# Optimization experiments

Measured on AMD Instinct MI355X. Metric: run time of the kernel, lower is better.

The kernel has to match this reference:

```python
import jax, jax.numpy as jnp
from jax import lax
import numpy as np

B, N, NPOINT, NSAMPLE = 4, 8192, 1024, 32
RADIUS = 0.2
EPS = 1e-5
C_IN = 16
MLP_DIMS = [(3 + C_IN, 64), (64, 64), (64, 128)]


def setup_inputs() -> dict:
    key = jax.random.key(0)
    ks = jax.random.split(key, 16)
    inp = {
        "xyz": jax.random.uniform(ks[0], (B, N, 3), dtype=jnp.float32),
        "points": jax.random.normal(ks[1], (B, N, C_IN), dtype=jnp.float32),
    }
    for i, (cin, cout) in enumerate(MLP_DIMS, 1):
        inp[f"w{i}"] = jax.random.normal(ks[1 + i], (cout, cin), dtype=jnp.float32) / np.sqrt(cin)
        inp[f"b{i}"] = jnp.zeros((cout,), jnp.float32)
        inp[f"g{i}"] = jnp.ones((cout,), jnp.float32)
        inp[f"be{i}"] = jnp.zeros((cout,), jnp.float32)
    return inp


def fps(xyz, npoint):
    # Farthest point sampling; sequential by nature -> lax.scan over npoint steps.
    # Deterministic start at index 0 (torch version uses a random start).
    b, n, _ = xyz.shape
    def step(carry, _):
        dist, far = carry
        centroid = jnp.take_along_axis(xyz, far[:, None, None], axis=1)  # [B,1,3]
        d = jnp.sum((xyz - centroid) ** 2, -1)                            # [B,N]
        dist = jnp.minimum(dist, d)
        return (dist, jnp.argmax(dist, -1).astype(jnp.int32)), far
    init = (jnp.full((b, n), 1e10, xyz.dtype), jnp.zeros((b,), jnp.int32))
    _, idxs = lax.scan(step, init, None, length=npoint)
    return jnp.transpose(idxs)  # [B, npoint]


def gather2(pts, idx):  # pts [B,N,C], idx [B,S] -> [B,S,C]
    return jnp.take_along_axis(pts, idx[..., None], axis=1)


def gather3(pts, idx):  # pts [B,N,C], idx [B,S,K] -> [B,S,K,C]
    b, s, k = idx.shape
    out = jnp.take_along_axis(pts, idx.reshape(b, s * k)[..., None], axis=1)
    return out.reshape(b, s, k, pts.shape[-1])


def ball_query(radius, nsample, xyz, new_xyz):
    n = xyz.shape[1]
    # [B,S,N] pairwise squared distances (the memory-bound hot spot)
    sqr = jnp.sum((new_xyz[:, :, None, :] - xyz[:, None, :, :]) ** 2, -1)
    gidx = jnp.where(sqr > radius * radius, n, jnp.arange(n, dtype=jnp.int32))
    gidx = jnp.sort(gidx, axis=-1)[:, :, :nsample]
    first = gidx[:, :, :1]
    return jnp.where(gidx == n, first, gidx)


def mlp_layer(x, w, b, g, be):
    # 1x1 Conv2d + BatchNorm2d (train mode: batch stats over B,S,K) + ReLU
    y = jnp.einsum('bskc,oc->bsko', x, w) + b
    mu = jnp.mean(y, axis=(0, 1, 2))
    var = jnp.var(y, axis=(0, 1, 2))
    y = (y - mu) * (g * lax.rsqrt(var + EPS)) + be
    return jax.nn.relu(y)


def reference(xyz, points, w1, b1, g1, be1, w2, b2, g2, be2, w3, b3, g3, be3):
    fps_idx = fps(xyz, NPOINT)                       # [B,S]
    new_xyz = gather2(xyz, fps_idx)                  # [B,S,3]
    idx = ball_query(RADIUS, NSAMPLE, xyz, new_xyz)  # [B,S,K]
    grouped_xyz_norm = gather3(xyz, idx) - new_xyz[:, :, None, :]  # [B,S,K,3]
    grouped_points = gather3(points, idx)            # [B,S,K,C]
    feat = jnp.concatenate([grouped_xyz_norm, grouped_points], -1)  # [B,S,K,3+C]
    feat = mlp_layer(feat, w1, b1, g1, be1)
    feat = mlp_layer(feat, w2, b2, g2, be2)
    feat = mlp_layer(feat, w3, b3, g3, be3)
    new_points = jnp.max(feat, axis=2)               # max-pool over neighbors -> [B,S,128]
    return new_xyz, new_points
```

## Files before the change

### kernel.cpp

```cpp
#include <hip/hip_runtime.h>

#define NB 4
#define NP 8192
#define NS 1024
#define NK 32
#define CNT_ALL 131072.0f

typedef float v2f __attribute__((ext_vector_type(2)));

template <int CTRL>
__device__ __forceinline__ unsigned dpp_max_u32(unsigned m)
{
    unsigned o = (unsigned)__builtin_amdgcn_update_dpp((int)m, (int)m, CTRL, 0xF, 0xF, false);
    return (o > m) ? o : m;
}

template <int CTRL>
__device__ __forceinline__ unsigned long long dpp_max_u64(unsigned long long k)
{
    unsigned lo = (unsigned)k, hi = (unsigned)(k >> 32);
    unsigned olo = (unsigned)__builtin_amdgcn_update_dpp((int)lo, (int)lo, CTRL, 0xF, 0xF, false);
    unsigned ohi = (unsigned)__builtin_amdgcn_update_dpp((int)hi, (int)hi, CTRL, 0xF, 0xF, false);
    unsigned long long o = ((unsigned long long)ohi << 32) | (unsigned long long)olo;
    return (o > k) ? o : k;
}

__global__ __launch_bounds__(512, 2) void fps_kernel(const float* __restrict__ xyz,
                                                     float* __restrict__ newxyz,
                                                     float* __restrict__ st)
{
#pragma clang fp contract(off)
    if (blockIdx.x >= NB) {
        for (int i = threadIdx.x; i < 4096; i += 512) st[i] = 0.f;
        return;
    }
    const int b = blockIdx.x;
    const int tid = threadIdx.x;
    const int lane = tid & 63;
    const int w = tid >> 6;
    const float* xb = xyz + (size_t)b * NP * 3;

    __shared__ float4 s_p4[NP];
    __shared__ unsigned long long s_kv[2][8];

#pragma unroll
    for (int k = 0; k < 16; ++k) {
        const int i = k * 512 + tid;
        s_p4[i] = make_float4(xb[3 * i + 0], xb[3 * i + 1], xb[3 * i + 2], 0.f);
    }
    __syncthreads();

    v2f px[8], py[8], pz[8], dist[8];
    const int base = tid << 4;
#pragma unroll
    for (int m = 0; m < 8; ++m) {
        const int p0 = base + 2 * m;
        const float4 a = s_p4[p0];
        const float4 c = s_p4[p0 + 1];
        px[m] = v2f{a.x, c.x};
        py[m] = v2f{a.y, c.y};
        pz[m] = v2f{a.z, c.z};
        dist[m] = v2f{1e10f, 1e10f};
    }
    float cx = s_p4[0].x, cy = s_p4[0].y, cz = s_p4[0].z;
    float* ob = newxyz + (size_t)b * NS * 3;

    for (int it = 0; it < NS; ++it) {
        if (tid == 0) { ob[it * 3 + 0] = cx; ob[it * 3 + 1] = cy; ob[it * 3 + 2] = cz; }
        const v2f cxx = v2f{cx, cx}, cyy = v2f{cy, cy}, czz = v2f{cz, cz};
        v2f bdv = v2f{-1.0f, -1.0f};
#pragma unroll
        for (int m = 0; m < 8; ++m) {
            v2f dx = px[m] - cxx, dy = py[m] - cyy, dz = pz[m] - czz;
            v2f d = (dx * dx + dy * dy) + dz * dz;
            v2f dj = __builtin_elementwise_min(dist[m], d);
            dist[m] = dj;
            bdv = __builtin_elementwise_max(bdv, dj);
        }
        const float bd = fmaxf(bdv.x, bdv.y);
        const unsigned ub = __float_as_uint(bd);
        unsigned m0 = dpp_max_u32<0xB1>(ub);
        m0 = dpp_max_u32<0x4E>(m0);
        m0 = dpp_max_u32<0x141>(m0);
        m0 = dpp_max_u32<0x140>(m0);
        m0 = dpp_max_u32<0x142>(m0);
        m0 = dpp_max_u32<0x143>(m0);
        const unsigned maxbits = (unsigned)__builtin_amdgcn_readlane((int)m0, 63);
        const unsigned long long bm = __ballot(ub == maxbits);
        const int srclane = __ffsll(bm) - 1;
        if (lane == srclane) {
            int j = 0;
#pragma unroll
            for (int m = 7; m >= 0; --m) {
                if (dist[m].y == bd) j = 2 * m + 1;
                if (dist[m].x == bd) j = 2 * m;
            }
            const int wbi = base + j;
            s_kv[it & 1][w] = ((unsigned long long)maxbits << 32)
                            | (unsigned)(NP - 1 - wbi);
        }
        __syncthreads();
        unsigned long long kv = s_kv[it & 1][lane & 7];
        kv = dpp_max_u64<0xB1>(kv);
        kv = dpp_max_u64<0x4E>(kv);
        kv = dpp_max_u64<0x141>(kv);
        const int fi = NP - 1 - (int)(unsigned)(kv & 0xFFFFFFFFull);
        const float4 c4 = s_p4[fi];
        cx = c4.x; cy = c4.y; cz = c4.z;
    }
}

__device__ __forceinline__ void bn_coef(const float* __restrict__ sums,
                                        const float* __restrict__ sqs,
                                        const float* __restrict__ g,
                                        const float* __restrict__ be,
                                        int C, int c, float& sc, float& sh)
{
    float s = 0.f, q = 0.f;
#pragma unroll
    for (int k = 0; k < 8; ++k) { s += sums[k * C + c]; q += sqs[k * C + c]; }
    const float mean = s / CNT_ALL;
    const float var = q / CNT_ALL - mean * mean;
    sc = g[c] / sqrtf(var + 1e-5f);
    sh = be[c] - mean * sc;
}

__global__ __launch_bounds__(256) void phaseA_kernel(
    const float* __restrict__ xyz, const float* __restrict__ pts,
    const float* __restrict__ newxyz,
    const float* __restrict__ w1, const float* __restrict__ b1,
    float* __restrict__ y1, float* __restrict__ st)
{
    __shared__ int   s_ball[8][NK];
    __shared__ float s_feat[256][20];
    __shared__ float s_ps[256], s_pq[256];
    float* sums1 = st;
    float* sqs1 = st + 512;

    const int tid = threadIdx.x;
    const int bk = blockIdx.x;
    const int lane = tid & 63;
    const int wv_id = tid >> 6;

    const int b = (8 * bk) >> 10;
    const float* xb = xyz + (size_t)b * NP * 3;
    const float rr = (float)(0.2 * 0.2);
    for (int r = 0; r < 2; ++r) {
        const int lg = 2 * wv_id + r;
        const int sg = 8 * bk + lg;
        const float cx = newxyz[sg * 3 + 0];
        const float cy = newxyz[sg * 3 + 1];
        const float cz = newxyz[sg * 3 + 2];
        int cnt = 0;
        for (int base = 0; base < NP && cnt < NK; base += 64) {
            const int p = base + lane;
            float dx = xb[p * 3 + 0] - cx;
            float dy = xb[p * 3 + 1] - cy;
            float dz = xb[p * 3 + 2] - cz;
            float d = __fadd_rn(__fadd_rn(__fmul_rn(dx, dx), __fmul_rn(dy, dy)),
                                __fmul_rn(dz, dz));
            bool in = (d <= rr);
            unsigned long long mask = __ballot(in);
            int before = __popcll(mask & ((1ull << lane) - 1ull));
            int pos = cnt + before;
            if (in && pos < NK) s_ball[lg][pos] = p;
            cnt += (int)__popcll(mask);
        }
        cnt = min(cnt, NK);
        const int v0 = s_ball[lg][0];
        if (lane < NK && lane >= cnt) s_ball[lg][lane] = v0;
    }
    __syncthreads();
    {
        const int lg = tid >> 5, k = tid & 31;
        const int id = s_ball[lg][k];
        const int sg = 8 * bk + lg;
        const float* pp = xyz + ((size_t)b * NP + id) * 3;
        const float* cp = newxyz + (size_t)sg * 3;
        float* f = s_feat[tid];
        f[0] = pp[0] - cp[0];
        f[1] = pp[1] - cp[1];
        f[2] = pp[2] - cp[2];
        const float4* q4 = (const float4*)(pts + ((size_t)b * NP + id) * 16);
#pragma unroll
        for (int i = 0; i < 4; ++i) {
            float4 v = q4[i];
            f[3 + 4 * i + 0] = v.x; f[3 + 4 * i + 1] = v.y;
            f[3 + 4 * i + 2] = v.z; f[3 + 4 * i + 3] = v.w;
        }
        f[19] = 0.f;
    }
    __syncthreads();
    const int c = tid & 63, rg = tid >> 6;
    float wv[20];
#pragma unroll
    for (int j = 0; j < 19; ++j) wv[j] = w1[c * 19 + j];
    wv[19] = 0.f;
    const float bs = b1[c];
    float s = 0.f, q = 0.f;
    for (int r = 0; r < 64; ++r) {
        const int row = rg * 64 + r;
        const float4* f4 = (const float4*)s_feat[row];
        float acc = bs;
#pragma unroll
        for (int j4 = 0; j4 < 5; ++j4) {
            float4 v = f4[j4];
            acc += wv[4*j4+0]*v.x + wv[4*j4+1]*v.y + wv[4*j4+2]*v.z + wv[4*j4+3]*v.w;
        }
        y1[((size_t)256 * bk + row) * 64 + c] = acc;
        s += acc; q += acc * acc;
    }
    s_ps[tid] = s; s_pq[tid] = q;
    __syncthreads();
    if (rg == 0) {
        float ts = s_ps[c] + s_ps[64 + c] + s_ps[128 + c] + s_ps[192 + c];
        float tq = s_pq[c] + s_pq[64 + c] + s_pq[128 + c] + s_pq[192 + c];
        atomicAdd(&sums1[(bk & 7) * 64 + c], ts);
        atomicAdd(&sqs1[(bk & 7) * 64 + c], tq);
    }
}

__global__ __launch_bounds__(256) void phaseB_kernel(
    const float* __restrict__ y1,
    const float* __restrict__ g1, const float* __restrict__ be1,
    const float* __restrict__ w2, const float* __restrict__ b2,
    float* __restrict__ y2, float* __restrict__ st)
{
    __shared__ float x_lds[128 * 64];
    __shared__ float s_sc[64], s_sh[64];
    __shared__ float s_ps[256], s_pq[256];
    const float* sums1 = st;
    const float* sqs1 = st + 512;
    float* sums2 = st + 1024;
    float* sqs2 = st + 1536;

    const int tid = threadIdx.x;
    const int bk = blockIdx.x;
    if (tid < 64) {
        float sc, sh;
        bn_coef(sums1, sqs1, g1, be1, 64, tid, sc, sh);
        s_sc[tid] = sc; s_sh[tid] = sh;
    }
    __syncthreads();
    const int c = tid & 63, rg = tid >> 6;
    float wv[64];
#pragma unroll
    for (int j = 0; j < 64; ++j) wv[j] = w2[c * 64 + j];
    const float bs = b2[c];
    float s = 0.f, q = 0.f;
    for (int half = 0; half < 2; ++half) {
        const size_t row0 = (size_t)256 * bk + 128 * half;
        const float4* y1g = (const float4*)(y1 + row0 * 64);
        float4* xl4 = (float4*)x_lds;
#pragma unroll
        for (int i = 0; i < 8; ++i) {
            const int slot = i * 256 + tid;
            float4 v = y1g[slot];
            const int c4 = (slot & 15) * 4;
            float4 o;
            o.x = fmaxf(v.x * s_sc[c4+0] + s_sh[c4+0], 0.f);
            o.y = fmaxf(v.y * s_sc[c4+1] + s_sh[c4+1], 0.f);
            o.z = fmaxf(v.z * s_sc[c4+2] + s_sh[c4+2], 0.f);
            o.w = fmaxf(v.w * s_sc[c4+3] + s_sh[c4+3], 0.f);
            xl4[slot] = o;
        }
        __syncthreads();
        for (int r = 0; r < 32; ++r) {
            const int row = rg * 32 + r;
            const float4* x4 = (const float4*)(x_lds + row * 64);
            float acc = bs;
#pragma unroll
            for (int j4 = 0; j4 < 16; ++j4) {
                float4 v = x4[j4];
                acc += wv[4*j4+0]*v.x + wv[4*j4+1]*v.y + wv[4*j4+2]*v.z + wv[4*j4+3]*v.w;
            }
            y2[(row0 + row) * 64 + c] = acc;
            s += acc; q += acc * acc;
        }
        __syncthreads();
    }
    s_ps[tid] = s; s_pq[tid] = q;
    __syncthreads();
    if (rg == 0) {
        float ts = s_ps[c] + s_ps[64 + c] + s_ps[128 + c] + s_ps[192 + c];
        float tq = s_pq[c] + s_pq[64 + c] + s_pq[128 + c] + s_pq[192 + c];
        atomicAdd(&sums2[(bk & 7) * 64 + c], ts);
        atomicAdd(&sqs2[(bk & 7) * 64 + c], tq);
    }
}

__global__ __launch_bounds__(256) void phaseC_kernel(
    const float* __restrict__ y2,
    const float* __restrict__ g2, const float* __restrict__ be2,
    const float* __restrict__ w3, const float* __restrict__ b3,
    float* __restrict__ st)
{
    __shared__ float s_x[NK * 64];
    __shared__ float s_sc[64], s_sh[64];
    __shared__ float s_p3s[256], s_p3q[256];
    const float* sums2 = st + 1024;
    const float* sqs2 = st + 1536;
    float* sums3 = st + 2048;
    float* sqs3 = st + 3072;

    const int tid = threadIdx.x;
    const int bk = blockIdx.x;
    if (tid < 64) {
        float sc, sh;
        bn_coef(sums2, sqs2, g2, be2, 64, tid, sc, sh);
        s_sc[tid] = sc; s_sh[tid] = sh;
    }
    __syncthreads();
    const int c = tid & 127, rg = tid >> 7;
    float wv[64];
#pragma unroll
    for (int j = 0; j < 64; ++j) wv[j] = w3[c * 64 + j];
    const float bs = b3[c];
    float s = 0.f, q = 0.f;
    for (int gi = 0; gi < 8; ++gi) {
        const size_t grow0 = (size_t)256 * bk + 32 * gi;
        const float4* y2g = (const float4*)(y2 + grow0 * 64);
        float4* sx4 = (float4*)s_x;
#pragma unroll
        for (int i = 0; i < 2; ++i) {
            const int slot = i * 256 + tid;
            float4 v = y2g[slot];
            const int c4 = (slot & 15) * 4;
            float4 o;
            o.x = fmaxf(v.x * s_sc[c4+0] + s_sh[c4+0], 0.f);
            o.y = fmaxf(v.y * s_sc[c4+1] + s_sh[c4+1], 0.f);
            o.z = fmaxf(v.z * s_sc[c4+2] + s_sh[c4+2], 0.f);
            o.w = fmaxf(v.w * s_sc[c4+3] + s_sh[c4+3], 0.f);
            sx4[slot] = o;
        }
        __syncthreads();
        for (int r = 0; r < 16; ++r) {
            const int row = rg * 16 + r;
            const float4* x4 = (const float4*)(s_x + row * 64);
            float acc = bs;
#pragma unroll
            for (int j4 = 0; j4 < 16; ++j4) {
                float4 v = x4[j4];
                acc += wv[4*j4+0]*v.x + wv[4*j4+1]*v.y + wv[4*j4+2]*v.z + wv[4*j4+3]*v.w;
            }
            s += acc; q += acc * acc;
        }
        __syncthreads();
    }
    s_p3s[rg * 128 + c] = s; s_p3q[rg * 128 + c] = q;
    __syncthreads();
    if (rg == 0) {
        atomicAdd(&sums3[(bk & 7) * 128 + c], s_p3s[c] + s_p3s[128 + c]);
        atomicAdd(&sqs3[(bk & 7) * 128 + c], s_p3q[c] + s_p3q[128 + c]);
    }
}

__global__ __launch_bounds__(256) void phaseD_kernel(
    const float* __restrict__ y2,
    const float* __restrict__ g2, const float* __restrict__ be2,
    const float* __restrict__ g3, const float* __restrict__ be3,
    const float* __restrict__ w3, const float* __restrict__ b3,
    const float* __restrict__ st, float* __restrict__ out_np)
{
    __shared__ float s_x[NK * 64];
    __shared__ float s_sc[64], s_sh[64];
    __shared__ float s_fm[256];
    const float* sums2 = st + 1024;
    const float* sqs2 = st + 1536;
    const float* sums3 = st + 2048;
    const float* sqs3 = st + 3072;

    const int tid = threadIdx.x;
    const int bk = blockIdx.x;
    if (tid < 64) {
        float sc, sh;
        bn_coef(sums2, sqs2, g2, be2, 64, tid, sc, sh);
        s_sc[tid] = sc; s_sh[tid] = sh;
    }
    const int c = tid & 127, rg = tid >> 7;
    float sc3, sh3;
    bn_coef(sums3, sqs3, g3, be3, 128, c, sc3, sh3);
    __syncthreads();
    float wv[64];
#pragma unroll
    for (int j = 0; j < 64; ++j) wv[j] = w3[c * 64 + j];
    const float bs = b3[c];
    for (int gi = 0; gi < 8; ++gi) {
        const size_t grow0 = (size_t)256 * bk + 32 * gi;
        const float4* y2g = (const float4*)(y2 + grow0 * 64);
        float4* sx4 = (float4*)s_x;
#pragma unroll
        for (int i = 0; i < 2; ++i) {
            const int slot = i * 256 + tid;
            float4 v = y2g[slot];
            const int c4 = (slot & 15) * 4;
            float4 o;
            o.x = fmaxf(v.x * s_sc[c4+0] + s_sh[c4+0], 0.f);
            o.y = fmaxf(v.y * s_sc[c4+1] + s_sh[c4+1], 0.f);
            o.z = fmaxf(v.z * s_sc[c4+2] + s_sh[c4+2], 0.f);
            o.w = fmaxf(v.w * s_sc[c4+3] + s_sh[c4+3], 0.f);
            sx4[slot] = o;
        }
        __syncthreads();
        float m = 0.f;
        for (int r = 0; r < 16; ++r) {
            const int row = rg * 16 + r;
            const float4* x4 = (const float4*)(s_x + row * 64);
            float acc = bs;
#pragma unroll
            for (int j4 = 0; j4 < 16; ++j4) {
                float4 v = x4[j4];
                acc += wv[4*j4+0]*v.x + wv[4*j4+1]*v.y + wv[4*j4+2]*v.z + wv[4*j4+3]*v.w;
            }
            float rv = fmaxf(acc * sc3 + sh3, 0.f);
            m = fmaxf(m, rv);
        }
        s_fm[rg * 128 + c] = m;
        __syncthreads();
        if (rg == 0)
            out_np[(size_t)(8 * bk + gi) * 128 + c] = fmaxf(s_fm[c], s_fm[128 + c]);
        __syncthreads();
    }
}

extern "C" void kernel_launch(void* const* d_in, const int* in_sizes, int n_in,
                              void* d_out, int out_size, void* d_ws, size_t ws_size,
                              hipStream_t stream)
{
    (void)in_sizes; (void)n_in; (void)out_size;
    const float* xyz = (const float*)d_in[0];
    const float* pts = (const float*)d_in[1];
    const float* w1 = (const float*)d_in[2];
    const float* b1 = (const float*)d_in[3];
    const float* g1 = (const float*)d_in[4];
    const float* be1 = (const float*)d_in[5];
    const float* w2 = (const float*)d_in[6];
    const float* b2 = (const float*)d_in[7];
    const float* g2 = (const float*)d_in[8];
    const float* be2 = (const float*)d_in[9];
    const float* w3 = (const float*)d_in[10];
    const float* b3 = (const float*)d_in[11];
    const float* g3 = (const float*)d_in[12];
    const float* be3 = (const float*)d_in[13];

    float* out = (float*)d_out;
    float* newxyz = out;
    float* newpts = out + NB * NS * 3;

    float* y1 = (float*)d_ws;
    float* y2 = y1 + 8388608;
    float* st = y2 + 8388608;
    const size_t needed = (2ull * 8388608ull + 4096ull) * 4ull;
    if (ws_size < needed) return;

    fps_kernel<<<NB + 1, 512, 0, stream>>>(xyz, newxyz, st);
    phaseA_kernel<<<512, 256, 0, stream>>>(xyz, pts, newxyz, w1, b1, y1, st);
    phaseB_kernel<<<512, 256, 0, stream>>>(y1, g1, be1, w2, b2, y2, st);
    phaseC_kernel<<<512, 256, 0, stream>>>(y2, g2, be2, w3, b3, st);
    phaseD_kernel<<<512, 256, 0, stream>>>(y2, g2, be2, g3, be3, w3, b3, st, newpts);
}
```

Baseline: 1.239 ms.

## Morton-sort points in FPS and skip distance updates for distant thread clusters

The FPS kernel now sorts each batch's points by Morton code with an in-shared-memory bitonic sort, so each thread owns 16 spatially clustered points. Each thread also computes a bounding sphere for its points. When a new centroid is far enough away that it cannot lower that thread's current maximum distance, the thread skips its distance update. The argmax key packs distance, original index and sorted slot so ties still resolve to the lowest original index. This removes per-iteration arithmetic for most threads, at the cost of a one-time sort, 64-bit reductions and lower occupancy (launch bounds 512,1).

Result: slower. 1.531 ms (+23.6%).

```diff
diff --git a/kernel.cpp b/kernel.cpp
--- a/kernel.cpp
+++ b/kernel.cpp
@@ -6,26 +6,29 @@
 #define NK 32
 #define CNT_ALL 131072.0f
 
-typedef float v2f __attribute__((ext_vector_type(2)));
+typedef unsigned long long u64;
 
 template <int CTRL>
-__device__ __forceinline__ unsigned dpp_max_u32(unsigned m)
-{
-    unsigned o = (unsigned)__builtin_amdgcn_update_dpp((int)m, (int)m, CTRL, 0xF, 0xF, false);
-    return (o > m) ? o : m;
-}
-
-template <int CTRL>
-__device__ __forceinline__ unsigned long long dpp_max_u64(unsigned long long k)
+__device__ __forceinline__ u64 dpp_max_u64(u64 k)
 {
     unsigned lo = (unsigned)k, hi = (unsigned)(k >> 32);
     unsigned olo = (unsigned)__builtin_amdgcn_update_dpp((int)lo, (int)lo, CTRL, 0xF, 0xF, false);
     unsigned ohi = (unsigned)__builtin_amdgcn_update_dpp((int)hi, (int)hi, CTRL, 0xF, 0xF, false);
-    unsigned long long o = ((unsigned long long)ohi << 32) | (unsigned long long)olo;
+    u64 o = ((u64)ohi << 32) | (u64)olo;
     return (o > k) ? o : k;
 }
 
-__global__ __launch_bounds__(512, 2) void fps_kernel(const float* __restrict__ xyz,
+__device__ __forceinline__ unsigned expand10(unsigned v)
+{
+    v &= 1023u;
+    v = (v | (v << 16)) & 0x030000FFu;
+    v = (v | (v << 8))  & 0x0300F00Fu;
+    v = (v | (v << 4))  & 0x030C30C3u;
+    v = (v | (v << 2))  & 0x09249249u;
+    return v;
+}
+
+__global__ __launch_bounds__(512, 1) void fps_kernel(const float* __restrict__ xyz,
                                                      float* __restrict__ newxyz,
                                                      float* __restrict__ st)
 {
@@ -34,78 +37,129 @@
         for (int i = threadIdx.x; i < 4096; i += 512) st[i] = 0.f;
         return;
     }
+    __shared__ __align__(16) char smem[131072 + 128];
+    u64*    keys = (u64*)smem;
+    float4* s_p4 = (float4*)smem;
+    u64*    s_kv = (u64*)(smem + 131072);
+
     const int b = blockIdx.x;
     const int tid = threadIdx.x;
     const int lane = tid & 63;
     const int w = tid >> 6;
     const float* xb = xyz + (size_t)b * NP * 3;
 
-    __shared__ float4 s_p4[NP];
-    __shared__ unsigned long long s_kv[2][8];
-
-#pragma unroll
     for (int k = 0; k < 16; ++k) {
         const int i = k * 512 + tid;
-        s_p4[i] = make_float4(xb[3 * i + 0], xb[3 * i + 1], xb[3 * i + 2], 0.f);
-    }
-    __syncthreads();
-
-    v2f px[8], py[8], pz[8], dist[8];
+        const float x = xb[3 * i + 0], y = xb[3 * i + 1], z = xb[3 * i + 2];
+        const unsigned ix = min((unsigned)(x * 1024.f), 1023u);
+        const unsigned iy = min((unsigned)(y * 1024.f), 1023u);
+        const unsigned iz = min((unsigned)(z * 1024.f), 1023u);
+        const unsigned mc = (expand10(ix) << 2) | (expand10(iy) << 1) | expand10(iz);
+        keys[i] = ((u64)mc << 13) | (unsigned)i;
+    }
+    __syncthreads();
+
+    for (int k = 2; k <= NP; k <<= 1) {
+        for (int j = k >> 1; j > 0; j >>= 1) {
+#pragma unroll
+            for (int u = 0; u < 8; ++u) {
+                const int idx = u * 512 + tid;
+                const int low = idx & (j - 1);
+                const int i = ((idx ^ low) << 1) | low;
+                const int p = i | j;
+                const bool up = ((i & k) == 0);
+                const u64 a = keys[i], bb = keys[p];
+                if ((a > bb) == up) { keys[i] = bb; keys[p] = a; }
+            }
+            __syncthreads();
+        }
+    }
+
     const int base = tid << 4;
-#pragma unroll
-    for (int m = 0; m < 8; ++m) {
-        const int p0 = base + 2 * m;
-        const float4 a = s_p4[p0];
-        const float4 c = s_p4[p0 + 1];
-        px[m] = v2f{a.x, c.x};
-        py[m] = v2f{a.y, c.y};
-        pz[m] = v2f{a.z, c.z};
-        dist[m] = v2f{1e10f, 1e10f};
-    }
-    float cx = s_p4[0].x, cy = s_p4[0].y, cz = s_p4[0].z;
+    u64 myk[16];
+#pragma unroll
+    for (int j = 0; j < 16; ++j) myk[j] = keys[base + j];
+    __syncthreads();
+
+    int oidx[16];
+    float px[16], py[16], pz[16], dist[16];
+#pragma unroll
+    for (int j = 0; j < 16; ++j) {
+        const int oi = (int)(myk[j] & 0x1FFFu);
+        oidx[j] = oi;
+        const float x = xb[3 * oi + 0], y = xb[3 * oi + 1], z = xb[3 * oi + 2];
+        px[j] = x; py[j] = y; pz[j] = z;
+        dist[j] = 1e10f;
+        s_p4[base + j] = make_float4(x, y, z, 0.f);
+    }
+    __syncthreads();
+
+    float mnx = px[0], mxx = px[0], mny = py[0], mxy = py[0], mnz = pz[0], mxz = pz[0];
+#pragma unroll
+    for (int j = 1; j < 16; ++j) {
+        mnx = fminf(mnx, px[j]); mxx = fmaxf(mxx, px[j]);
+        mny = fminf(mny, py[j]); mxy = fmaxf(mxy, py[j]);
+        mnz = fminf(mnz, pz[j]); mxz = fmaxf(mxz, pz[j]);
+    }
+    const float cmx = (mnx + mxx) * 0.5f;
+    const float cmy = (mny + mxy) * 0.5f;
+    const float cmz = (mnz + mxz) * 0.5f;
+    float r2 = 0.f;
+#pragma unroll
+    for (int j = 0; j < 16; ++j) {
+        const float dx = px[j] - cmx, dy = py[j] - cmy, dz = pz[j] - cmz;
+        r2 = fmaxf(r2, dx * dx + dy * dy + dz * dz);
+    }
+    const float rb = sqrtf(r2) * 1.000002f + 1e-7f;
+
+    u64 key = ((u64)0x7F800000u << 26);
+    float cx = xb[0], cy = xb[1], cz = xb[2];
     float* ob = newxyz + (size_t)b * NS * 3;
 
     for (int it = 0; it < NS; ++it) {
         if (tid == 0) { ob[it * 3 + 0] = cx; ob[it * 3 + 1] = cy; ob[it * 3 + 2] = cz; }
-        const v2f cxx = v2f{cx, cx}, cyy = v2f{cy, cy}, czz = v2f{cz, cz};
-        v2f bdv = v2f{-1.0f, -1.0f};
-#pragma unroll
-        for (int m = 0; m < 8; ++m) {
-            v2f dx = px[m] - cxx, dy = py[m] - cyy, dz = pz[m] - czz;
-            v2f d = (dx * dx + dy * dy) + dz * dz;
-            v2f dj = __builtin_elementwise_min(dist[m], d);
-            dist[m] = dj;
-            bdv = __builtin_elementwise_max(bdv, dj);
-        }
-        const float bd = fmaxf(bdv.x, bdv.y);
-        const unsigned ub = __float_as_uint(bd);
-        unsigned m0 = dpp_max_u32<0xB1>(ub);
-        m0 = dpp_max_u32<0x4E>(m0);
-        m0 = dpp_max_u32<0x141>(m0);
-        m0 = dpp_max_u32<0x140>(m0);
-        m0 = dpp_max_u32<0x142>(m0);
-        m0 = dpp_max_u32<0x143>(m0);
-        const unsigned maxbits = (unsigned)__builtin_amdgcn_readlane((int)m0, 63);
-        const unsigned long long bm = __ballot(ub == maxbits);
-        const int srclane = __ffsll(bm) - 1;
-        if (lane == srclane) {
-            int j = 0;
-#pragma unroll
-            for (int m = 7; m >= 0; --m) {
-                if (dist[m].y == bd) j = 2 * m + 1;
-                if (dist[m].x == bd) j = 2 * m;
+        const float ddx = cx - cmx, ddy = cy - cmy, ddz = cz - cmz;
+        const float t = sqrtf(ddx * ddx + ddy * ddy + ddz * ddz);
+        const float s = t - rb - 1e-5f;
+        const float Mt = __uint_as_float((unsigned)(key >> 26));
+        const bool skip = (s > 0.f) && (s * s >= Mt);
+        if (!skip) {
+            float bd = -1.f;
+#pragma unroll
+            for (int j = 0; j < 16; ++j) {
+                const float dx = px[j] - cx, dy = py[j] - cy, dz = pz[j] - cz;
+                const float d = (dx * dx + dy * dy) + dz * dz;
+                const float dj = fminf(dist[j], d);
+                dist[j] = dj;
+                bd = fmaxf(bd, dj);
             }
-            const int wbi = base + j;
-            s_kv[it & 1][w] = ((unsigned long long)maxbits << 32)
-                            | (unsigned)(NP - 1 - wbi);
-        }
-        __syncthreads();
-        unsigned long long kv = s_kv[it & 1][lane & 7];
+            int bo = 0x7FFFFFFF, bs = 0;
+#pragma unroll
+            for (int j = 0; j < 16; ++j) {
+                const bool e = (dist[j] == bd) && (oidx[j] < bo);
+                bo = e ? oidx[j] : bo;
+                bs = e ? (base + j) : bs;
+            }
+            key = ((u64)__float_as_uint(bd) << 26) | ((u64)(unsigned)(8191 - bo) << 13)
+                | (unsigned)bs;
+        }
+        u64 wk = dpp_max_u64<0xB1>(key);
+        wk = dpp_max_u64<0x4E>(wk);
+        wk = dpp_max_u64<0x141>(wk);
+        wk = dpp_max_u64<0x140>(wk);
+        wk = dpp_max_u64<0x142>(wk);
+        wk = dpp_max_u64<0x143>(wk);
+        const unsigned wlo = (unsigned)__builtin_amdgcn_readlane((int)(unsigned)wk, 63);
+        const unsigned whi = (unsigned)__builtin_amdgcn_readlane((int)(unsigned)(wk >> 32), 63);
+        const u64 wmax = ((u64)whi << 32) | wlo;
+        if (key == wmax) s_kv[(it & 1) * 8 + w] = wmax;
+        __syncthreads();
+        u64 kv = s_kv[(it & 1) * 8 + (lane & 7)];
         kv = dpp_max_u64<0xB1>(kv);
         kv = dpp_max_u64<0x4E>(kv);
         kv = dpp_max_u64<0x141>(kv);
-        const int fi = NP - 1 - (int)(unsigned)(kv & 0xFFFFFFFFull);
-        const float4 c4 = s_p4[fi];
+        const int fs = (int)(kv & 0x1FFFu);
+        const float4 c4 = s_p4[fs];
         cx = c4.x; cy = c4.y; cz = c4.z;
     }
 }
```
